# Kernel tuning notes

Measured on AMD Instinct MI355X. Metric: run time of the kernel, lower is better.

## Reference

```python
import jax, jax.numpy as jnp
import numpy as np

D_MODEL = 1024
N_HEADS = 16
HEAD_DIM = D_MODEL // N_HEADS
ROPE_DIM = HEAD_DIM  # rope_fraction=1.0
BASE = 10000.0


def _rope_cos_sin(T, dtype):
    theta = 1.0 / (BASE ** (jnp.arange(0, ROPE_DIM, 2, dtype=jnp.float32) / ROPE_DIM))
    t = jnp.arange(T, dtype=jnp.float32)
    freqs = jnp.outer(t, theta)                     # [T, ROPE_DIM/2]
    emb = jnp.concatenate([freqs, freqs], axis=-1)  # [T, ROPE_DIM]
    return jnp.cos(emb).astype(dtype), jnp.sin(emb).astype(dtype)


def _rotate(x, cos, sin):
    # x: [B, H, T, D]; apply rotary to first ROPE_DIM dims (here full D)
    x_rope, x_pass = x[..., :ROPE_DIM], x[..., ROPE_DIM:]
    x1, x2 = x_rope[..., :ROPE_DIM // 2], x_rope[..., ROPE_DIM // 2:]
    rotated = jnp.concatenate([-x2, x1], axis=-1)
    x_rope = x_rope * cos + rotated * sin
    return jnp.concatenate([x_rope, x_pass], axis=-1)


def setup_inputs() -> dict:
    key = jax.random.key(0)
    k1, k2, k3 = jax.random.split(key, 3)
    x = jax.random.normal(k1, (4, 2048, D_MODEL), dtype=jnp.float32)
    w_qkv = jax.random.normal(k2, (3 * D_MODEL, D_MODEL), dtype=jnp.float32) * (1.0 / np.sqrt(D_MODEL))
    w_out = jax.random.normal(k3, (D_MODEL, D_MODEL), dtype=jnp.float32) * (1.0 / np.sqrt(D_MODEL))
    return {"x": x, "w_qkv": w_qkv, "w_out": w_out}


def reference(x, w_qkv, w_out):
    B, T, C = x.shape
    qkv = jnp.einsum('btc,oc->bto', x, w_qkv)  # Linear: x @ W.T
    q, k, v = jnp.split(qkv, 3, axis=-1)

    def reshape(t):
        return t.reshape(B, T, N_HEADS, HEAD_DIM).transpose(0, 2, 1, 3)  # [B,H,T,D]

    q, k, v = reshape(q), reshape(k), reshape(v)

    cos, sin = _rope_cos_sin(T, x.dtype)  # [T, ROPE_DIM]
    cos = cos[None, None, :, :]
    sin = sin[None, None, :, :]
    q = _rotate(q, cos, sin)
    k = _rotate(k, cos, sin)

    scale = 1.0 / np.sqrt(HEAD_DIM).astype(np.float32)
    attn = jnp.einsum('bhqd,bhkd->bhqk', q, k) * scale
    causal = jnp.tril(jnp.ones((T, T), dtype=bool))
    attn = jnp.where(causal[None, None], attn, jnp.finfo(attn.dtype).min)
    attn = jax.nn.softmax(attn, axis=-1)
    out = jnp.einsum('bhqk,bhkd->bhqd', attn, v)
    out = out.transpose(0, 2, 1, 3).reshape(B, T, C)
    return jnp.einsum('btc,oc->bto', out, w_out)
```

## Files before the change

kernel.cpp:

```cpp
#include <hip/hip_runtime.h>

typedef unsigned short u16;
typedef __attribute__((ext_vector_type(8))) short v8s;
typedef __attribute__((ext_vector_type(4))) float v4f;

__device__ __forceinline__ u16 f2bf(float f) {
  unsigned u = __float_as_uint(f);
  u += 0x7FFF + ((u >> 16) & 1);
  return (u16)(u >> 16);
}

__device__ __forceinline__ unsigned pk2bf(float lo, float hi) {
  unsigned a = __float_as_uint(lo) + 0x8000u;
  unsigned b = __float_as_uint(hi) + 0x8000u;
  return __builtin_amdgcn_perm(b, a, 0x07060302);
}

__device__ __forceinline__ v4f zero4() {
  v4f z; z[0] = 0.f; z[1] = 0.f; z[2] = 0.f; z[3] = 0.f; return z;
}

__device__ __forceinline__ void async16(const u16* g, u16* l) {
  __builtin_amdgcn_global_load_lds(
      (const __attribute__((address_space(1))) unsigned int*)g,
      (__attribute__((address_space(3))) unsigned int*)l, 16, 0, 0);
}

__device__ __forceinline__ void fast_sincos(float x, float* s, float* c) {
  float k = rintf(x * 0.15915494309189535f);
  float r = __builtin_fmaf(k, -6.28125f, x);
  r = __builtin_fmaf(k, -0.0019353071795864769f, r);
  *s = __sinf(r);
  *c = __cosf(r);
}

#define ATTN_SCL (0.125f * 1.4426950408889634f)

__global__ __launch_bounds__(256) void cast_all_k(const float* __restrict__ x,
                                                  const float* __restrict__ wq,
                                                  const float* __restrict__ wo,
                                                  u16* __restrict__ dst) {
  int i = blockIdx.x * 256 + threadIdx.x;
  const float4* s;
  int si;
  if (i < 2097152) { s = (const float4*)x;  si = i; }
  else if (i < 2883584) { s = (const float4*)wq; si = i - 2097152; }
  else { s = (const float4*)wo; si = i - 2883584; }
  float4 v = s[si];
  ((ushort4*)dst)[i] = make_ushort4(f2bf(v.x), f2bf(v.y), f2bf(v.z), f2bf(v.w));
}


__device__ __forceinline__ void gemm_core(const u16* __restrict__ A,
                                          const u16* __restrict__ B, int K,
                                          int row0, int col0, u16* As, u16* Bs,
                                          v4f acc[4][4]) {
  const int tid = threadIdx.x;
  const int lane = tid & 63;
  const int wm = (tid >> 7) & 1;
  const int wn = (tid >> 6) & 1;
  const int ln = lane & 15, quad = lane >> 4;
#pragma unroll
  for (int i = 0; i < 4; ++i)
#pragma unroll
    for (int j = 0; j < 4; ++j) acc[i][j] = zero4();
  const int rA = tid >> 3;
  const int cA = (((tid & 7) ^ (rA & 7)) << 3);
  for (int kt = 0; kt < K; kt += 64) {
#pragma unroll
    for (int i = 0; i < 4; ++i) {
      async16(A + (size_t)(row0 + i * 32 + rA) * K + kt + cA, As + i * 2048 + tid * 8);
      async16(B + (size_t)(col0 + i * 32 + rA) * K + kt + cA, Bs + i * 2048 + tid * 8);
    }
    __syncthreads();
#pragma unroll
    for (int kk = 0; kk < 2; ++kk) {
      const int go = (((kk * 4 + quad) ^ (ln & 7)) << 3);
      v8s af[4], bfr[4];
#pragma unroll
      for (int i = 0; i < 4; ++i) {
        af[i]  = *(const v8s*)(As + (wm * 64 + i * 16 + ln) * 64 + go);
        bfr[i] = *(const v8s*)(Bs + (wn * 64 + i * 16 + ln) * 64 + go);
      }
      __builtin_amdgcn_s_setprio(1);
#pragma unroll
      for (int i = 0; i < 4; ++i)
#pragma unroll
        for (int j = 0; j < 4; ++j)
          acc[i][j] = __builtin_amdgcn_mfma_f32_16x16x32_bf16(af[i], bfr[j], acc[i][j], 0, 0, 0);
      __builtin_amdgcn_s_setprio(0);
    }
    __syncthreads();
  }
}

__global__ __launch_bounds__(256) void gemm_qkv_rope(const u16* __restrict__ A,
                                                     const u16* __restrict__ B,
                                                     u16* __restrict__ Qh,
                                                     u16* __restrict__ Kh,
                                                     u16* __restrict__ Vt) {
  __shared__ __align__(16) u16 As[8192];
  __shared__ __align__(16) u16 Bs[8192];
  v4f acc[4][4];
  const int row0 = blockIdx.x * 128, col0 = blockIdx.y * 128;
  gemm_core(A, B, 1024, row0, col0, As, Bs, acc);
  const int tid = threadIdx.x, lane = tid & 63;
  const int wm = (tid >> 7) & 1, wn = (tid >> 6) & 1;
  const int ln = lane & 15, quad = lane >> 4;
  const int colbase = col0 + wn * 64;
  const int seg = colbase >> 10;
  const int h = (colbase & 1023) >> 6;
  if (seg < 2) {
    u16* dst = (seg == 0) ? Qh : Kh;
    const float oscl = (seg == 0) ? ATTN_SCL : 1.0f;
#pragma unroll
    for (int i = 0; i < 4; ++i) {
#pragma unroll
      for (int r = 0; r < 4; ++r) {
        int row = row0 + wm * 64 + i * 16 + quad * 4 + r;
        int b = row >> 11, t = row & 2047;
        size_t base = ((size_t)(b * 16 + h) * 2048 + t) * 64;
#pragma unroll
        for (int j = 0; j < 2; ++j) {
          int d1 = j * 16 + ln;
          float theta = exp2f((float)d1 * -0.4152410118609203f);
          float sn, cs;
          fast_sincos((float)t * theta, &sn, &cs);
          float v1 = acc[i][j][r], v2 = acc[i][j + 2][r];
          dst[base + d1]      = f2bf((v1 * cs - v2 * sn) * oscl);
          dst[base + d1 + 32] = f2bf((v2 * cs + v1 * sn) * oscl);
        }
      }
    }
  } else {
#pragma unroll
    for (int i = 0; i < 4; ++i)
#pragma unroll
      for (int j = 0; j < 4; ++j) {
        int d = j * 16 + ln;
#pragma unroll
        for (int r = 0; r < 4; ++r) {
          int row = row0 + wm * 64 + i * 16 + quad * 4 + r;
          int b = row >> 11, t = row & 2047;
          Vt[((size_t)(b * 16 + h) * 64 + d) * 2048 + t] = f2bf(acc[i][j][r]);
        }
      }
  }
}

__global__ __launch_bounds__(256, 4) void gemm_out_k(const u16* __restrict__ A,
                                                     const u16* __restrict__ B,
                                                     float* __restrict__ C) {
  __shared__ __align__(16) u16 As[128 * 64];
  __shared__ __align__(16) u16 Bs[64 * 64];
  const int tid = threadIdx.x;
  const int lane = tid & 63;
  const int wm = (tid >> 7) & 1;
  const int wn = (tid >> 6) & 1;
  const int ln = lane & 15, quad = lane >> 4;
  const int row0 = blockIdx.x * 128, col0 = blockIdx.y * 64;
  const int K = 1024;
  v4f acc[4][2];
#pragma unroll
  for (int i = 0; i < 4; ++i)
#pragma unroll
    for (int j = 0; j < 2; ++j) acc[i][j] = zero4();
  const int rA = tid >> 3;
  const int cA = (((tid & 7) ^ (rA & 7)) << 3);
  for (int kt = 0; kt < K; kt += 64) {
#pragma unroll
    for (int i = 0; i < 4; ++i)
      async16(A + (size_t)(row0 + i * 32 + rA) * K + kt + cA, As + i * 2048 + tid * 8);
#pragma unroll
    for (int i = 0; i < 2; ++i)
      async16(B + (size_t)(col0 + i * 32 + rA) * K + kt + cA, Bs + i * 2048 + tid * 8);
    __syncthreads();
#pragma unroll
    for (int kk = 0; kk < 2; ++kk) {
      const int go = (((kk * 4 + quad) ^ (ln & 7)) << 3);
      v8s af[4], bfr[2];
#pragma unroll
      for (int i = 0; i < 4; ++i)
        af[i] = *(const v8s*)(As + (wm * 64 + i * 16 + ln) * 64 + go);
#pragma unroll
      for (int j = 0; j < 2; ++j)
        bfr[j] = *(const v8s*)(Bs + (wn * 32 + j * 16 + ln) * 64 + go);
      __builtin_amdgcn_s_setprio(1);
#pragma unroll
      for (int i = 0; i < 4; ++i)
#pragma unroll
        for (int j = 0; j < 2; ++j)
          acc[i][j] = __builtin_amdgcn_mfma_f32_16x16x32_bf16(af[i], bfr[j], acc[i][j], 0, 0, 0);
      __builtin_amdgcn_s_setprio(0);
    }
    __syncthreads();
  }
#pragma unroll
  for (int i = 0; i < 4; ++i)
#pragma unroll
    for (int r = 0; r < 4; ++r) {
      int row = row0 + wm * 64 + i * 16 + quad * 4 + r;
#pragma unroll
      for (int j = 0; j < 2; ++j) {
        int col = col0 + wn * 32 + j * 16 + ln;
        C[(size_t)row * 1024 + col] = acc[i][j][r];
      }
    }
}


template <bool MASKED>
__device__ __forceinline__ void qk_sm_pv(const v8s ak[2][4], const v8s av[2][4],
                                         u16* Pw, const v8s aq[2], v4f od[4],
                                         float& l, int s0, int qrow, int ln,
                                         int quad, int swz) {
  v4f sc[4];
#pragma unroll
  for (int kf = 0; kf < 4; ++kf) sc[kf] = zero4();
#pragma unroll
  for (int kk = 0; kk < 2; ++kk) {
    __builtin_amdgcn_s_setprio(1);
#pragma unroll
    for (int kf = 0; kf < 4; ++kf)
      sc[kf] = __builtin_amdgcn_mfma_f32_16x16x32_bf16(ak[kk][kf], aq[kk], sc[kf], 0, 0, 0);
    __builtin_amdgcn_s_setprio(0);
  }
  float ls = 0.f;
#pragma unroll
  for (int kf = 0; kf < 4; ++kf) {
    float p[4];
#pragma unroll
    for (int r = 0; r < 4; ++r) {
      float v = sc[kf][r];
      if (MASKED) {
        int key = s0 + kf * 16 + quad * 4 + r;
        v = (key <= qrow) ? v : -3.0e38f;
      }
      p[r] = exp2f(v);
    }
    ls += (p[0] + p[1]) + (p[2] + p[3]);
    uint2 pk;
    pk.x = pk2bf(p[0], p[1]);
    pk.y = pk2bf(p[2], p[3]);
    *(uint2*)(Pw + ln * 64 + (((kf * 4 + quad) ^ swz) << 2)) = pk;
  }
  l += ls;
#pragma unroll
  for (int kk = 0; kk < 2; ++kk) {
    v8s bp = *(const v8s*)(Pw + ln * 64 + (((kk * 8 + quad * 2) ^ swz) << 2));
    __builtin_amdgcn_s_setprio(1);
#pragma unroll
    for (int df = 0; df < 4; ++df)
      od[df] = __builtin_amdgcn_mfma_f32_16x16x32_bf16(av[kk][df], bp, od[df], 0, 0, 0);
    __builtin_amdgcn_s_setprio(0);
  }
}

__device__ __forceinline__ void flash_epi(float l, const v4f od[4], int t,
                                          int b, int h, int quad,
                                          u16* __restrict__ O) {
  float lt = l;
  lt += __shfl_xor(lt, 16);
  lt += __shfl_xor(lt, 32);
  float inv = 1.0f / lt;
  size_t obase = ((size_t)b * 2048 + t) * 1024 + h * 64;
#pragma unroll
  for (int df = 0; df < 4; ++df) {
    ushort4 o;
    o.x = f2bf(od[df][0] * inv);
    o.y = f2bf(od[df][1] * inv);
    o.z = f2bf(od[df][2] * inv);
    o.w = f2bf(od[df][3] * inv);
    *(ushort4*)(O + obase + df * 16 + quad * 4) = o;
  }
}

__global__ __launch_bounds__(256, 2) void flash_k(const u16* __restrict__ Q,
                                                  const u16* __restrict__ Kh,
                                                  const u16* __restrict__ V,
                                                  u16* __restrict__ O) {
  __shared__ __align__(16) u16 Ks[2][4096];
  __shared__ __align__(16) u16 Vs[2][4096];
  __shared__ __align__(16) u16 Ps[4096];
  const int tid = threadIdx.x;
  const int lane = tid & 63, w = tid >> 6;
  const int ln = lane & 15, quad = lane >> 4;
  const int swz = (lane & 7) << 1;
  const int by = blockIdx.y;
  const int bh = blockIdx.x;
  const int b = bh >> 4, h = bh & 15;
  const size_t qoff = (size_t)bh * 2048 * 64;
  u16* Pw = Ps + w * 1024;

  const int rS = tid >> 3;
  const int cS = (((tid & 7) ^ (rS & 7)) << 3);
  const u16* Kbase = Kh + qoff;
  const u16* Vbase = V + (size_t)bh * 131072;

#pragma unroll
  for (int ph = 0; ph < 2; ++ph) {
    const int qx = ph ? by : 15 - by;
    const int nt = 2 * qx + 2;
    const int diag = 2 * qx + (w >> 1);
    const int S0 = qx * 128 + w * 32;
    const int qrow0 = S0 + ln, qrow1 = S0 + 16 + ln;
    v8s aq0[2], aq1[2];
#pragma unroll
    for (int kk = 0; kk < 2; ++kk) {
      aq0[kk] = *(const v8s*)(Q + qoff + (size_t)(S0 + ln) * 64 + kk * 32 + quad * 8);
      aq1[kk] = *(const v8s*)(Q + qoff + (size_t)(S0 + 16 + ln) * 64 + kk * 32 + quad * 8);
    }
    float l0 = 0.f, l1 = 0.f;
    v4f od0[4], od1[4];
#pragma unroll
    for (int df = 0; df < 4; ++df) { od0[df] = zero4(); od1[df] = zero4(); }

    {
      async16(Kbase + (size_t)rS * 64 + cS, Ks[0] + tid * 8);
      async16(Kbase + (size_t)(32 + rS) * 64 + cS, Ks[0] + 2048 + tid * 8);
      async16(Vbase + (size_t)rS * 2048 + cS, Vs[0] + tid * 8);
      async16(Vbase + (size_t)(rS + 32) * 2048 + cS, Vs[0] + 2048 + tid * 8);
    }
    for (int it = 0; it < nt; ++it) {
      __syncthreads();
      if (it + 1 < nt) {
        const int s1 = (it + 1) * 64;
        u16* kd = Ks[(it + 1) & 1];
        u16* vd = Vs[(it + 1) & 1];
        async16(Kbase + (size_t)(s1 + rS) * 64 + cS, kd + tid * 8);
        async16(Kbase + (size_t)(s1 + 32 + rS) * 64 + cS, kd + 2048 + tid * 8);
        async16(Vbase + (size_t)rS * 2048 + s1 + cS, vd + tid * 8);
        async16(Vbase + (size_t)(rS + 32) * 2048 + s1 + cS, vd + 2048 + tid * 8);
      }
      if (it <= diag) {
        const u16* Kc = Ks[it & 1];
        const u16* Vc = Vs[it & 1];
        v8s ak[2][4], av[2][4];
#pragma unroll
        for (int kk = 0; kk < 2; ++kk) {
          const int go = (((kk * 4 + quad) ^ (ln & 7)) << 3);
#pragma unroll
          for (int i = 0; i < 4; ++i) {
            ak[kk][i] = *(const v8s*)(Kc + (i * 16 + ln) * 64 + go);
            av[kk][i] = *(const v8s*)(Vc + (i * 16 + ln) * 64 + go);
          }
        }
        const int s0 = it * 64;
        if (it == diag) {
          qk_sm_pv<true>(ak, av, Pw, aq0, od0, l0, s0, qrow0, ln, quad, swz);
          qk_sm_pv<true>(ak, av, Pw, aq1, od1, l1, s0, qrow1, ln, quad, swz);
        } else {
          qk_sm_pv<false>(ak, av, Pw, aq0, od0, l0, s0, qrow0, ln, quad, swz);
          qk_sm_pv<false>(ak, av, Pw, aq1, od1, l1, s0, qrow1, ln, quad, swz);
        }
      }
    }
    __syncthreads();

    flash_epi(l0, od0, S0 + ln, b, h, quad, O);
    flash_epi(l1, od1, S0 + 16 + ln, b, h, quad, O);
  }
}

extern "C" void kernel_launch(void* const* d_in, const int* in_sizes, int n_in,
                              void* d_out, int out_size, void* d_ws, size_t ws_size,
                              hipStream_t stream) {
  const float* x     = (const float*)d_in[0];
  const float* w_qkv = (const float*)d_in[1];
  const float* w_out = (const float*)d_in[2];
  float* out = (float*)d_out;
  char* ws = (char*)d_ws;
  u16* xb    = (u16*)(ws);
  u16* wqkvb = (u16*)(ws + 16777216);
  u16* woutb = (u16*)(ws + 23068672);
  u16* qh    = (u16*)(ws + 25165824);
  u16* kh    = (u16*)(ws + 41943040);
  u16* vt    = (u16*)(ws + 58720256);
  u16* oa    = (u16*)(ws + 75497472);

  cast_all_k<<<12288, 256, 0, stream>>>(x, w_qkv, w_out, (u16*)ws);
  gemm_qkv_rope<<<dim3(64, 24), 256, 0, stream>>>(xb, wqkvb, qh, kh, vt);
  flash_k<<<dim3(64, 8), 256, 0, stream>>>(qh, kh, vt, oa);
  gemm_out_k<<<dim3(64, 16), 256, 0, stream>>>(oa, woutb, out);
}
```

Baseline: 249.1 us.

## Split flash blocks to one query tile each and use shared GEMM core for out-proj

```diff
diff --git a/kernel.cpp b/kernel.cpp
--- a/kernel.cpp
+++ b/kernel.cpp
@@ -148,61 +148,25 @@
   }
 }
 
-__global__ __launch_bounds__(256, 4) void gemm_out_k(const u16* __restrict__ A,
-                                                     const u16* __restrict__ B,
-                                                     float* __restrict__ C) {
-  __shared__ __align__(16) u16 As[128 * 64];
-  __shared__ __align__(16) u16 Bs[64 * 64];
-  const int tid = threadIdx.x;
-  const int lane = tid & 63;
-  const int wm = (tid >> 7) & 1;
-  const int wn = (tid >> 6) & 1;
+__global__ __launch_bounds__(256) void gemm_out_k(const u16* __restrict__ A,
+                                                  const u16* __restrict__ B,
+                                                  float* __restrict__ C) {
+  __shared__ __align__(16) u16 As[8192];
+  __shared__ __align__(16) u16 Bs[8192];
+  v4f acc[4][4];
+  const int row0 = blockIdx.x * 128, col0 = blockIdx.y * 128;
+  gemm_core(A, B, 1024, row0, col0, As, Bs, acc);
+  const int tid = threadIdx.x, lane = tid & 63;
+  const int wm = (tid >> 7) & 1, wn = (tid >> 6) & 1;
   const int ln = lane & 15, quad = lane >> 4;
-  const int row0 = blockIdx.x * 128, col0 = blockIdx.y * 64;
-  const int K = 1024;
-  v4f acc[4][2];
-#pragma unroll
-  for (int i = 0; i < 4; ++i)
-#pragma unroll
-    for (int j = 0; j < 2; ++j) acc[i][j] = zero4();
-  const int rA = tid >> 3;
-  const int cA = (((tid & 7) ^ (rA & 7)) << 3);
-  for (int kt = 0; kt < K; kt += 64) {
-#pragma unroll
-    for (int i = 0; i < 4; ++i)
-      async16(A + (size_t)(row0 + i * 32 + rA) * K + kt + cA, As + i * 2048 + tid * 8);
-#pragma unroll
-    for (int i = 0; i < 2; ++i)
-      async16(B + (size_t)(col0 + i * 32 + rA) * K + kt + cA, Bs + i * 2048 + tid * 8);
-    __syncthreads();
-#pragma unroll
-    for (int kk = 0; kk < 2; ++kk) {
-      const int go = (((kk * 4 + quad) ^ (ln & 7)) << 3);
-      v8s af[4], bfr[2];
-#pragma unroll
-      for (int i = 0; i < 4; ++i)
-        af[i] = *(const v8s*)(As + (wm * 64 + i * 16 + ln) * 64 + go);
-#pragma unroll
-      for (int j = 0; j < 2; ++j)
-        bfr[j] = *(const v8s*)(Bs + (wn * 32 + j * 16 + ln) * 64 + go);
-      __builtin_amdgcn_s_setprio(1);
-#pragma unroll
-      for (int i = 0; i < 4; ++i)
-#pragma unroll
-        for (int j = 0; j < 2; ++j)
-          acc[i][j] = __builtin_amdgcn_mfma_f32_16x16x32_bf16(af[i], bfr[j], acc[i][j], 0, 0, 0);
-      __builtin_amdgcn_s_setprio(0);
-    }
-    __syncthreads();
-  }
 #pragma unroll
   for (int i = 0; i < 4; ++i)
 #pragma unroll
     for (int r = 0; r < 4; ++r) {
       int row = row0 + wm * 64 + i * 16 + quad * 4 + r;
 #pragma unroll
-      for (int j = 0; j < 2; ++j) {
-        int col = col0 + wn * 32 + j * 16 + ln;
+      for (int j = 0; j < 4; ++j) {
+        int col = col0 + wn * 64 + j * 16 + ln;
         C[(size_t)row * 1024 + col] = acc[i][j][r];
       }
     }
@@ -286,7 +250,7 @@
   const int lane = tid & 63, w = tid >> 6;
   const int ln = lane & 15, quad = lane >> 4;
   const int swz = (lane & 7) << 1;
-  const int by = blockIdx.y;
+  const int qx = 15 - blockIdx.y;
   const int bh = blockIdx.x;
   const int b = bh >> 4, h = bh & 15;
   const size_t qoff = (size_t)bh * 2048 * 64;
@@ -297,69 +261,64 @@
   const u16* Kbase = Kh + qoff;
   const u16* Vbase = V + (size_t)bh * 131072;
 
-#pragma unroll
-  for (int ph = 0; ph < 2; ++ph) {
-    const int qx = ph ? by : 15 - by;
-    const int nt = 2 * qx + 2;
-    const int diag = 2 * qx + (w >> 1);
-    const int S0 = qx * 128 + w * 32;
-    const int qrow0 = S0 + ln, qrow1 = S0 + 16 + ln;
-    v8s aq0[2], aq1[2];
-#pragma unroll
-    for (int kk = 0; kk < 2; ++kk) {
-      aq0[kk] = *(const v8s*)(Q + qoff + (size_t)(S0 + ln) * 64 + kk * 32 + quad * 8);
-      aq1[kk] = *(const v8s*)(Q + qoff + (size_t)(S0 + 16 + ln) * 64 + kk * 32 + quad * 8);
-    }
-    float l0 = 0.f, l1 = 0.f;
-    v4f od0[4], od1[4];
-#pragma unroll
-    for (int df = 0; df < 4; ++df) { od0[df] = zero4(); od1[df] = zero4(); }
-
-    {
-      async16(Kbase + (size_t)rS * 64 + cS, Ks[0] + tid * 8);
-      async16(Kbase + (size_t)(32 + rS) * 64 + cS, Ks[0] + 2048 + tid * 8);
-      async16(Vbase + (size_t)rS * 2048 + cS, Vs[0] + tid * 8);
-      async16(Vbase + (size_t)(rS + 32) * 2048 + cS, Vs[0] + 2048 + tid * 8);
-    }
-    for (int it = 0; it < nt; ++it) {
-      __syncthreads();
-      if (it + 1 < nt) {
-        const int s1 = (it + 1) * 64;
-        u16* kd = Ks[(it + 1) & 1];
-        u16* vd = Vs[(it + 1) & 1];
-        async16(Kbase + (size_t)(s1 + rS) * 64 + cS, kd + tid * 8);
-        async16(Kbase + (size_t)(s1 + 32 + rS) * 64 + cS, kd + 2048 + tid * 8);
-        async16(Vbase + (size_t)rS * 2048 + s1 + cS, vd + tid * 8);
-        async16(Vbase + (size_t)(rS + 32) * 2048 + s1 + cS, vd + 2048 + tid * 8);
-      }
-      if (it <= diag) {
-        const u16* Kc = Ks[it & 1];
-        const u16* Vc = Vs[it & 1];
-        v8s ak[2][4], av[2][4];
-#pragma unroll
-        for (int kk = 0; kk < 2; ++kk) {
-          const int go = (((kk * 4 + quad) ^ (ln & 7)) << 3);
-#pragma unroll
-          for (int i = 0; i < 4; ++i) {
-            ak[kk][i] = *(const v8s*)(Kc + (i * 16 + ln) * 64 + go);
-            av[kk][i] = *(const v8s*)(Vc + (i * 16 + ln) * 64 + go);
-          }
+  const int nt = 2 * qx + 2;
+  const int diag = 2 * qx + (w >> 1);
+  const int S0 = qx * 128 + w * 32;
+  const int qrow0 = S0 + ln, qrow1 = S0 + 16 + ln;
+  v8s aq0[2], aq1[2];
+#pragma unroll
+  for (int kk = 0; kk < 2; ++kk) {
+    aq0[kk] = *(const v8s*)(Q + qoff + (size_t)(S0 + ln) * 64 + kk * 32 + quad * 8);
+    aq1[kk] = *(const v8s*)(Q + qoff + (size_t)(S0 + 16 + ln) * 64 + kk * 32 + quad * 8);
+  }
+  float l0 = 0.f, l1 = 0.f;
+  v4f od0[4], od1[4];
+#pragma unroll
+  for (int df = 0; df < 4; ++df) { od0[df] = zero4(); od1[df] = zero4(); }
+
+  {
+    async16(Kbase + (size_t)rS * 64 + cS, Ks[0] + tid * 8);
+    async16(Kbase + (size_t)(32 + rS) * 64 + cS, Ks[0] + 2048 + tid * 8);
+    async16(Vbase + (size_t)rS * 2048 + cS, Vs[0] + tid * 8);
+    async16(Vbase + (size_t)(rS + 32) * 2048 + cS, Vs[0] + 2048 + tid * 8);
+  }
+  for (int it = 0; it < nt; ++it) {
+    __syncthreads();
+    if (it + 1 < nt) {
+      const int s1 = (it + 1) * 64;
+      u16* kd = Ks[(it + 1) & 1];
+      u16* vd = Vs[(it + 1) & 1];
+      async16(Kbase + (size_t)(s1 + rS) * 64 + cS, kd + tid * 8);
+      async16(Kbase + (size_t)(s1 + 32 + rS) * 64 + cS, kd + 2048 + tid * 8);
+      async16(Vbase + (size_t)rS * 2048 + s1 + cS, vd + tid * 8);
+      async16(Vbase + (size_t)(rS + 32) * 2048 + s1 + cS, vd + 2048 + tid * 8);
+    }
+    if (it <= diag) {
+      const u16* Kc = Ks[it & 1];
+      const u16* Vc = Vs[it & 1];
+      v8s ak[2][4], av[2][4];
+#pragma unroll
+      for (int kk = 0; kk < 2; ++kk) {
+        const int go = (((kk * 4 + quad) ^ (ln & 7)) << 3);
+#pragma unroll
+        for (int i = 0; i < 4; ++i) {
+          ak[kk][i] = *(const v8s*)(Kc + (i * 16 + ln) * 64 + go);
+          av[kk][i] = *(const v8s*)(Vc + (i * 16 + ln) * 64 + go);
         }
-        const int s0 = it * 64;
-        if (it == diag) {
-          qk_sm_pv<true>(ak, av, Pw, aq0, od0, l0, s0, qrow0, ln, quad, swz);
-          qk_sm_pv<true>(ak, av, Pw, aq1, od1, l1, s0, qrow1, ln, quad, swz);
-        } else {
-          qk_sm_pv<false>(ak, av, Pw, aq0, od0, l0, s0, qrow0, ln, quad, swz);
-          qk_sm_pv<false>(ak, av, Pw, aq1, od1, l1, s0, qrow1, ln, quad, swz);
-        }
-      }
-    }
-    __syncthreads();
-
-    flash_epi(l0, od0, S0 + ln, b, h, quad, O);
-    flash_epi(l1, od1, S0 + 16 + ln, b, h, quad, O);
-  }
+      }
+      const int s0 = it * 64;
+      if (it == diag) {
+        qk_sm_pv<true>(ak, av, Pw, aq0, od0, l0, s0, qrow0, ln, quad, swz);
+        qk_sm_pv<true>(ak, av, Pw, aq1, od1, l1, s0, qrow1, ln, quad, swz);
+      } else {
+        qk_sm_pv<false>(ak, av, Pw, aq0, od0, l0, s0, qrow0, ln, quad, swz);
+        qk_sm_pv<false>(ak, av, Pw, aq1, od1, l1, s0, qrow1, ln, quad, swz);
+      }
+    }
+  }
+
+  flash_epi(l0, od0, S0 + ln, b, h, quad, O);
+  flash_epi(l1, od1, S0 + 16 + ln, b, h, quad, O);
 }
 
 extern "C" void kernel_launch(void* const* d_in, const int* in_sizes, int n_in,
@@ -380,6 +339,6 @@
 
   cast_all_k<<<12288, 256, 0, stream>>>(x, w_qkv, w_out, (u16*)ws);
   gemm_qkv_rope<<<dim3(64, 24), 256, 0, stream>>>(xb, wqkvb, qh, kh, vt);
-  flash_k<<<dim3(64, 8), 256, 0, stream>>>(qh, kh, vt, oa);
-  gemm_out_k<<<dim3(64, 16), 256, 0, stream>>>(oa, woutb, out);
-}
+  flash_k<<<dim3(64, 16), 256, 0, stream>>>(qh, kh, vt, oa);
+  gemm_out_k<<<dim3(64, 8), 256, 0, stream>>>(oa, woutb, out);
+}
```

Measured after the change: 246.5 us, median of 2. Within noise of the previous version (-1.0%).

## Stage V transpose through LDS and split flash blocks per query tile

Applied to the files above, without the earlier changes.

```diff
diff --git a/kernel.cpp b/kernel.cpp
--- a/kernel.cpp
+++ b/kernel.cpp
@@ -99,8 +99,9 @@
                                                      u16* __restrict__ Qh,
                                                      u16* __restrict__ Kh,
                                                      u16* __restrict__ Vt) {
-  __shared__ __align__(16) u16 As[8192];
-  __shared__ __align__(16) u16 Bs[8192];
+  __shared__ __align__(16) u16 Ls[16384];
+  u16* As = Ls;
+  u16* Bs = Ls + 8192;
   v4f acc[4][4];
   const int row0 = blockIdx.x * 128, col0 = blockIdx.y * 128;
   gemm_core(A, B, 1024, row0, col0, As, Bs, acc);
@@ -137,14 +138,26 @@
     for (int i = 0; i < 4; ++i)
 #pragma unroll
       for (int j = 0; j < 4; ++j) {
-        int d = j * 16 + ln;
-#pragma unroll
-        for (int r = 0; r < 4; ++r) {
-          int row = row0 + wm * 64 + i * 16 + quad * 4 + r;
-          int b = row >> 11, t = row & 2047;
-          Vt[((size_t)(b * 16 + h) * 64 + d) * 2048 + t] = f2bf(acc[i][j][r]);
-        }
-      }
+        int dl = wn * 64 + j * 16 + ln;
+        int tb = wm * 64 + i * 16 + quad * 4;
+        int tS = tb ^ ((dl & 15) << 3);
+        unsigned lo = (unsigned)f2bf(acc[i][j][0]) | ((unsigned)f2bf(acc[i][j][1]) << 16);
+        unsigned hi = (unsigned)f2bf(acc[i][j][2]) | ((unsigned)f2bf(acc[i][j][3]) << 16);
+        *(uint2*)(Ls + dl * 128 + tS) = make_uint2(lo, hi);
+      }
+    __syncthreads();
+    const int dl = tid >> 1;
+    const int hh = ((col0 + dl) & 1023) >> 6;
+    const int din = dl & 63;
+    const int tb = (row0 & 2047) + (tid & 1) * 64;
+    const size_t vb = ((size_t)((row0 >> 11) * 16 + hh) * 64 + din) * 2048 + tb;
+    const int swz = (dl & 15) << 3;
+#pragma unroll
+    for (int c = 0; c < 8; ++c) {
+      int tl = (tid & 1) * 64 + c * 8;
+      v8s v = *(const v8s*)(Ls + dl * 128 + (tl ^ swz));
+      *(v8s*)(Vt + vb + c * 8) = v;
+    }
   }
 }
 
@@ -208,7 +221,6 @@
     }
 }
 
-
 template <bool MASKED>
 __device__ __forceinline__ void qk_sm_pv(const v8s ak[2][4], const v8s av[2][4],
                                          u16* Pw, const v8s aq[2], v4f od[4],
@@ -286,7 +298,7 @@
   const int lane = tid & 63, w = tid >> 6;
   const int ln = lane & 15, quad = lane >> 4;
   const int swz = (lane & 7) << 1;
-  const int by = blockIdx.y;
+  const int qx = 15 - blockIdx.y;
   const int bh = blockIdx.x;
   const int b = bh >> 4, h = bh & 15;
   const size_t qoff = (size_t)bh * 2048 * 64;
@@ -297,69 +309,64 @@
   const u16* Kbase = Kh + qoff;
   const u16* Vbase = V + (size_t)bh * 131072;
 
-#pragma unroll
-  for (int ph = 0; ph < 2; ++ph) {
-    const int qx = ph ? by : 15 - by;
-    const int nt = 2 * qx + 2;
-    const int diag = 2 * qx + (w >> 1);
-    const int S0 = qx * 128 + w * 32;
-    const int qrow0 = S0 + ln, qrow1 = S0 + 16 + ln;
-    v8s aq0[2], aq1[2];
-#pragma unroll
-    for (int kk = 0; kk < 2; ++kk) {
-      aq0[kk] = *(const v8s*)(Q + qoff + (size_t)(S0 + ln) * 64 + kk * 32 + quad * 8);
-      aq1[kk] = *(const v8s*)(Q + qoff + (size_t)(S0 + 16 + ln) * 64 + kk * 32 + quad * 8);
-    }
-    float l0 = 0.f, l1 = 0.f;
-    v4f od0[4], od1[4];
-#pragma unroll
-    for (int df = 0; df < 4; ++df) { od0[df] = zero4(); od1[df] = zero4(); }
-
-    {
-      async16(Kbase + (size_t)rS * 64 + cS, Ks[0] + tid * 8);
-      async16(Kbase + (size_t)(32 + rS) * 64 + cS, Ks[0] + 2048 + tid * 8);
-      async16(Vbase + (size_t)rS * 2048 + cS, Vs[0] + tid * 8);
-      async16(Vbase + (size_t)(rS + 32) * 2048 + cS, Vs[0] + 2048 + tid * 8);
-    }
-    for (int it = 0; it < nt; ++it) {
-      __syncthreads();
-      if (it + 1 < nt) {
-        const int s1 = (it + 1) * 64;
-        u16* kd = Ks[(it + 1) & 1];
-        u16* vd = Vs[(it + 1) & 1];
-        async16(Kbase + (size_t)(s1 + rS) * 64 + cS, kd + tid * 8);
-        async16(Kbase + (size_t)(s1 + 32 + rS) * 64 + cS, kd + 2048 + tid * 8);
-        async16(Vbase + (size_t)rS * 2048 + s1 + cS, vd + tid * 8);
-        async16(Vbase + (size_t)(rS + 32) * 2048 + s1 + cS, vd + 2048 + tid * 8);
-      }
-      if (it <= diag) {
-        const u16* Kc = Ks[it & 1];
-        const u16* Vc = Vs[it & 1];
-        v8s ak[2][4], av[2][4];
-#pragma unroll
-        for (int kk = 0; kk < 2; ++kk) {
-          const int go = (((kk * 4 + quad) ^ (ln & 7)) << 3);
-#pragma unroll
-          for (int i = 0; i < 4; ++i) {
-            ak[kk][i] = *(const v8s*)(Kc + (i * 16 + ln) * 64 + go);
-            av[kk][i] = *(const v8s*)(Vc + (i * 16 + ln) * 64 + go);
-          }
+  const int nt = 2 * qx + 2;
+  const int diag = 2 * qx + (w >> 1);
+  const int S0 = qx * 128 + w * 32;
+  const int qrow0 = S0 + ln, qrow1 = S0 + 16 + ln;
+  v8s aq0[2], aq1[2];
+#pragma unroll
+  for (int kk = 0; kk < 2; ++kk) {
+    aq0[kk] = *(const v8s*)(Q + qoff + (size_t)(S0 + ln) * 64 + kk * 32 + quad * 8);
+    aq1[kk] = *(const v8s*)(Q + qoff + (size_t)(S0 + 16 + ln) * 64 + kk * 32 + quad * 8);
+  }
+  float l0 = 0.f, l1 = 0.f;
+  v4f od0[4], od1[4];
+#pragma unroll
+  for (int df = 0; df < 4; ++df) { od0[df] = zero4(); od1[df] = zero4(); }
+
+  {
+    async16(Kbase + (size_t)rS * 64 + cS, Ks[0] + tid * 8);
+    async16(Kbase + (size_t)(32 + rS) * 64 + cS, Ks[0] + 2048 + tid * 8);
+    async16(Vbase + (size_t)rS * 2048 + cS, Vs[0] + tid * 8);
+    async16(Vbase + (size_t)(rS + 32) * 2048 + cS, Vs[0] + 2048 + tid * 8);
+  }
+  for (int it = 0; it < nt; ++it) {
+    __syncthreads();
+    if (it + 1 < nt) {
+      const int s1 = (it + 1) * 64;
+      u16* kd = Ks[(it + 1) & 1];
+      u16* vd = Vs[(it + 1) & 1];
+      async16(Kbase + (size_t)(s1 + rS) * 64 + cS, kd + tid * 8);
+      async16(Kbase + (size_t)(s1 + 32 + rS) * 64 + cS, kd + 2048 + tid * 8);
+      async16(Vbase + (size_t)rS * 2048 + s1 + cS, vd + tid * 8);
+      async16(Vbase + (size_t)(rS + 32) * 2048 + s1 + cS, vd + 2048 + tid * 8);
+    }
+    if (it <= diag) {
+      const u16* Kc = Ks[it & 1];
+      const u16* Vc = Vs[it & 1];
+      v8s ak[2][4], av[2][4];
+#pragma unroll
+      for (int kk = 0; kk < 2; ++kk) {
+        const int go = (((kk * 4 + quad) ^ (ln & 7)) << 3);
+#pragma unroll
+        for (int i = 0; i < 4; ++i) {
+          ak[kk][i] = *(const v8s*)(Kc + (i * 16 + ln) * 64 + go);
+          av[kk][i] = *(const v8s*)(Vc + (i * 16 + ln) * 64 + go);
         }
-        const int s0 = it * 64;
-        if (it == diag) {
-          qk_sm_pv<true>(ak, av, Pw, aq0, od0, l0, s0, qrow0, ln, quad, swz);
-          qk_sm_pv<true>(ak, av, Pw, aq1, od1, l1, s0, qrow1, ln, quad, swz);
-        } else {
-          qk_sm_pv<false>(ak, av, Pw, aq0, od0, l0, s0, qrow0, ln, quad, swz);
-          qk_sm_pv<false>(ak, av, Pw, aq1, od1, l1, s0, qrow1, ln, quad, swz);
-        }
-      }
-    }
-    __syncthreads();
-
-    flash_epi(l0, od0, S0 + ln, b, h, quad, O);
-    flash_epi(l1, od1, S0 + 16 + ln, b, h, quad, O);
-  }
+      }
+      const int s0 = it * 64;
+      if (it == diag) {
+        qk_sm_pv<true>(ak, av, Pw, aq0, od0, l0, s0, qrow0, ln, quad, swz);
+        qk_sm_pv<true>(ak, av, Pw, aq1, od1, l1, s0, qrow1, ln, quad, swz);
+      } else {
+        qk_sm_pv<false>(ak, av, Pw, aq0, od0, l0, s0, qrow0, ln, quad, swz);
+        qk_sm_pv<false>(ak, av, Pw, aq1, od1, l1, s0, qrow1, ln, quad, swz);
+      }
+    }
+  }
+
+  flash_epi(l0, od0, S0 + ln, b, h, quad, O);
+  flash_epi(l1, od1, S0 + 16 + ln, b, h, quad, O);
 }
 
 extern "C" void kernel_launch(void* const* d_in, const int* in_sizes, int n_in,
@@ -380,6 +387,6 @@
 
   cast_all_k<<<12288, 256, 0, stream>>>(x, w_qkv, w_out, (u16*)ws);
   gemm_qkv_rope<<<dim3(64, 24), 256, 0, stream>>>(xb, wqkvb, qh, kh, vt);
-  flash_k<<<dim3(64, 8), 256, 0, stream>>>(qh, kh, vt, oa);
+  flash_k<<<dim3(64, 16), 256, 0, stream>>>(qh, kh, vt, oa);
   gemm_out_k<<<dim3(64, 16), 256, 0, stream>>>(oa, woutb, out);
 }
```

After: 259.5 us. +4.2%, slower.
